# Kernel tuning notes

Hardware: AMD Instinct MI355X
Metric: run time of the kernel (lower is better)

The kernel has to match this reference:

```python
import jax, jax.numpy as jnp
import numpy as np

B, NQ, NK, D, H = 4, 2048, 2048, 1024, 16
HD = D // H


def setup_inputs() -> dict:
    key = jax.random.key(0)
    ks = jax.random.split(key, 11)
    s = 1.0 / np.sqrt(D)
    return {
        "q": jax.random.normal(ks[0], (B, NQ, D), jnp.float32),
        "k": jax.random.normal(ks[1], (B, NK, D), jnp.float32),
        "v": jax.random.normal(ks[2], (B, NK, D), jnp.float32),
        "Wq": jax.random.uniform(ks[3], (D, D), jnp.float32, -s, s),
        "bq": jax.random.uniform(ks[4], (D,), jnp.float32, -s, s),
        "Wk": jax.random.uniform(ks[5], (D, D), jnp.float32, -s, s),
        "bk": jax.random.uniform(ks[6], (D,), jnp.float32, -s, s),
        "Wv": jax.random.uniform(ks[7], (D, D), jnp.float32, -s, s),
        "bv": jax.random.uniform(ks[8], (D,), jnp.float32, -s, s),
        "Wo": jax.random.uniform(ks[9], (D, D), jnp.float32, -s, s),
        "bo": jax.random.uniform(ks[10], (D,), jnp.float32, -s, s),
    }


def reference(q, k, v, Wq, bq, Wk, bk, Wv, bv, Wo, bo):
    # Linear projections (torch Linear: x @ W.T + b), split into heads [B,H,N,HD]
    qh = (q @ Wq.T + bq).reshape(B, NQ, H, HD).transpose(0, 2, 1, 3)
    kh = (k @ Wk.T + bk).reshape(B, NK, H, HD).transpose(0, 2, 1, 3)
    vh = (v @ Wv.T + bv).reshape(B, NK, H, HD).transpose(0, 2, 1, 3)
    scores = jnp.einsum('bhqd,bhkd->bhqk', qh, kh) / np.sqrt(HD)  # [B,H,Nq,Nk]
    probs = jax.nn.softmax(scores, axis=-1)
    out = jnp.einsum('bhqk,bhkd->bhqd', probs, vh)
    out = out.transpose(0, 2, 1, 3).reshape(B, NQ, D)
    return out @ Wo.T + bo
```

## Files before the change

kernel.cpp:

```cpp
#include <hip/hip_runtime.h>
#include <hip/hip_bf16.h>
#include <cstdint>
#include <cstddef>


typedef __bf16 bf16x8 __attribute__((ext_vector_type(8)));
typedef float f32x4 __attribute__((ext_vector_type(4)));

#define BB 4
#define NQ 2048
#define NK 2048
#define DD 1024
#define HH 16
#define HD 64

#define QSCALE (0.125f * 1.4426950408889634f)

#if __has_builtin(__builtin_amdgcn_exp2f)
#define EXP2F(x) __builtin_amdgcn_exp2f(x)
#else
#define EXP2F(x) exp2f(x)
#endif

__device__ inline void gld_lds16(const void* g, void* lds) {
  __builtin_amdgcn_global_load_lds(
      (__attribute__((address_space(1))) unsigned int*)(g),
      (__attribute__((address_space(3))) unsigned int*)(lds),
      16, 0, 0);
}

__device__ inline bool probe_f32(const void* p) {
  const unsigned short* u = (const unsigned short*)p;
  int bad = 0;
#pragma unroll
  for (int i = 0; i < 64; ++i) {
    const int e = (u[2 * i] >> 7) & 0xFF;
    bad += (e > 0x8F) ? 1 : 0;
  }
  return bad >= 4;
}

__device__ inline bf16x8 cvt8(const float* src) {
  union { bf16x8 v; __hip_bfloat16 h[8]; } u;
#pragma unroll
  for (int j = 0; j < 8; ++j) u.h[j] = __float2bfloat16(src[j]);
  return u.v;
}

__global__ __launch_bounds__(256) void cvt_all(
    const void* __restrict__ q, const void* __restrict__ k,
    const void* __restrict__ v,
    const void* __restrict__ Wq, const void* __restrict__ Wk,
    const void* __restrict__ Wv, const void* __restrict__ Wo,
    __hip_bfloat16* __restrict__ qb, __hip_bfloat16* __restrict__ kb,
    __hip_bfloat16* __restrict__ vb, __hip_bfloat16* __restrict__ Wb) {
  const int bidx = blockIdx.x;
  const void* src; __hip_bfloat16* dst; size_t voff;
  if (bidx < 1536) {
    const int s = bidx >> 9;
    src = s == 0 ? q : (s == 1 ? k : v);
    dst = s == 0 ? qb : (s == 1 ? kb : vb);
    voff = (size_t)(bidx & 511) * 2048;
  } else {
    const int wi = (bidx - 1536) >> 6;
    src = wi == 0 ? Wq : (wi == 1 ? Wk : (wi == 2 ? Wv : Wo));
    dst = Wb + (size_t)wi * (DD * DD);
    voff = (size_t)((bidx - 1536) & 63) * 2048;
  }
  __shared__ int sflag;
  if (threadIdx.x == 0) sflag = probe_f32(src) ? 1 : 0;
  __syncthreads();
  const bool f32 = sflag != 0;
  const int t = threadIdx.x;
#pragma unroll
  for (int i = 0; i < 8; ++i) {
    const size_t j = voff + (size_t)i * 256 + t;
    if (f32) {
      union { f32x4 v2[2]; float f[8]; } u;
      const f32x4* s4 = (const f32x4*)src;
      u.v2[0] = s4[j * 2]; u.v2[1] = s4[j * 2 + 1];
      *(bf16x8*)(dst + j * 8) = cvt8(u.f);
    } else {
      *(f32x4*)(dst + j * 8) = ((const f32x4*)src)[j];
    }
  }
}

__global__ __launch_bounds__(256, 3) void gemm_fast(
    const __hip_bfloat16* __restrict__ qb, const __hip_bfloat16* __restrict__ kb,
    const __hip_bfloat16* __restrict__ vb, const __hip_bfloat16* __restrict__ At,
    const __hip_bfloat16* __restrict__ Wb,
    const void* __restrict__ bq, const void* __restrict__ bk,
    const void* __restrict__ bv, const void* __restrict__ bo,
    const void* __restrict__ WoOrig,
    void* __restrict__ Qp, void* __restrict__ Kp,
    void* __restrict__ Vt, void* __restrict__ Out, int cfg0) {
  __shared__ __align__(16) __hip_bfloat16 sA[2][128 * 32];
  __shared__ __align__(16) __hip_bfloat16 sB[2][128 * 32];
  const int t = threadIdx.x;
  const int wave = t >> 6, lane = t & 63;
  const int q4 = lane >> 4, c16 = lane & 15;
  const int wr = wave >> 1, wc = wave & 1;

  const int bid = blockIdx.x;
  const int xcd = bid & 7, idx = bid >> 3;
  const int z = idx >> 6;
  const int r6 = idx & 63;
  const int bm = xcd * 8 + (r6 >> 3);
  const int bn = r6 & 7;
  const int cfg = cfg0 + z;

  const __hip_bfloat16* A; const void* biasv; void* Cv; int mode; float scale = 1.f;
  if (cfg == 0)      { A = qb; biasv = bq; Cv = Qp; mode = 0; scale = QSCALE; }
  else if (cfg == 1) { A = kb; biasv = bk; Cv = Kp; mode = 0; }
  else if (cfg == 2) { A = vb; biasv = bv; Cv = Vt; mode = 1; }
  else               { A = At; biasv = bo; Cv = Out; mode = 2; }
  const __hip_bfloat16* Bm = Wb + (size_t)cfg * (DD * DD);

  const bool bias_f32 = probe_f32(biasv);
  const bool c_f32 = (mode == 2) && probe_f32(WoOrig);

  f32x4 acc[4][4];
#pragma unroll
  for (int i = 0; i < 4; ++i)
#pragma unroll
    for (int j = 0; j < 4; ++j) acc[i][j] = (f32x4){0.f, 0.f, 0.f, 0.f};

  const size_t baseA = (size_t)bm * 128 * DD;
  const size_t baseB = (size_t)bn * 128 * DD;
  const int po = ((q4) ^ (c16 & 3)) * 8;

  size_t offA[2], offB[2];
  int lslot[2];
#pragma unroll
  for (int i = 0; i < 2; ++i) {
    const int slot = i * 256 + t;
    const int row = slot >> 2, pg = (slot & 3) ^ (row & 3);
    lslot[i] = slot;
    offA[i] = baseA + (size_t)row * DD + pg * 8;
    offB[i] = baseB + (size_t)row * DD + pg * 8;
  }

#pragma unroll
  for (int i = 0; i < 2; ++i) {
    gld_lds16(A + offA[i], &sA[0][lslot[i] * 8]);
    gld_lds16(Bm + offB[i], &sB[0][lslot[i] * 8]);
  }
  __syncthreads();

  for (int it = 0; it < DD / 32; ++it) {
    const int p = it & 1;
    if (it + 1 < DD / 32) {
      const int koff = (it + 1) * 32;
#pragma unroll
      for (int i = 0; i < 2; ++i) {
        gld_lds16(A + offA[i] + koff, &sA[p ^ 1][lslot[i] * 8]);
        gld_lds16(Bm + offB[i] + koff, &sB[p ^ 1][lslot[i] * 8]);
      }
    }

    bf16x8 af[4], bfm[4];
#pragma unroll
    for (int rt = 0; rt < 4; ++rt)
      af[rt] = *(const bf16x8*)(&sA[p][0] + (wr * 64 + rt * 16 + c16) * 32 + po);
#pragma unroll
    for (int ct = 0; ct < 4; ++ct)
      bfm[ct] = *(const bf16x8*)(&sB[p][0] + (wc * 64 + ct * 16 + c16) * 32 + po);
#pragma unroll
    for (int rt = 0; rt < 4; ++rt)
#pragma unroll
      for (int ct = 0; ct < 4; ++ct)
        acc[rt][ct] = __builtin_amdgcn_mfma_f32_16x16x32_bf16(af[rt], bfm[ct],
                                                              acc[rt][ct], 0, 0, 0);

    __syncthreads();
  }

  const int row0 = bm * 128 + wr * 64 + q4 * 4;
  const int col0 = bn * 128 + wc * 64 + c16;
#pragma unroll
  for (int ct = 0; ct < 4; ++ct) {
    const int col = col0 + ct * 16;
    const float bvx = bias_f32 ? ((const float*)biasv)[col]
                               : __bfloat162float(((const __hip_bfloat16*)biasv)[col]);
#pragma unroll
    for (int rt = 0; rt < 4; ++rt) {
#pragma unroll
      for (int r = 0; r < 4; ++r) {
        const int row = row0 + rt * 16 + r;
        const float val = (acc[rt][ct][r] + bvx) * scale;
        if (mode == 1) {
          const int b = row >> 11, key = row & 2047;
          const int h = col >> 6, hd = col & 63;
          ((__hip_bfloat16*)Cv)[(size_t)((b * HH + h) * HD + hd) * NK + key] =
              __float2bfloat16(val);
        } else if (c_f32) {
          ((float*)Cv)[(size_t)row * DD + col] = val;
        } else {
          ((__hip_bfloat16*)Cv)[(size_t)row * DD + col] = __float2bfloat16(val);
        }
      }
    }
  }
}

__device__ inline void ld_slot(bool f32, const void* basep, size_t eoff,
                               f32x4& lo, f32x4& hi) {
  if (f32) {
    const f32x4* p = (const f32x4*)((const float*)basep + eoff);
    lo = p[0]; hi = p[1];
  } else {
    lo = *(const f32x4*)((const __hip_bfloat16*)basep + eoff);
  }
}

__device__ inline void st_slot(bool f32, __hip_bfloat16* dst, f32x4 lo, f32x4 hi) {
  if (f32) {
    union { f32x4 v[2]; float f[8]; } u;
    u.v[0] = lo; u.v[1] = hi;
    *(bf16x8*)dst = cvt8(u.f);
  } else {
    *(f32x4*)dst = lo;
  }
}

__global__ __launch_bounds__(256, 3) void gemm_mha(
    const void* __restrict__ qin, const void* __restrict__ kin,
    const void* __restrict__ vin, const void* __restrict__ ain,
    const void* __restrict__ Wq, const void* __restrict__ bq,
    const void* __restrict__ Wk, const void* __restrict__ bk,
    const void* __restrict__ Wv, const void* __restrict__ bv,
    const void* __restrict__ Wo, const void* __restrict__ bo,
    void* __restrict__ Qp, void* __restrict__ Kp,
    void* __restrict__ Vt, void* __restrict__ Out, int cfg0) {
  __shared__ __align__(16) __hip_bfloat16 sA[2][128 * 32];
  __shared__ __align__(16) __hip_bfloat16 sB[2][128 * 32];
  const int t = threadIdx.x;
  const int wave = t >> 6, lane = t & 63;
  const int q4 = lane >> 4, c16 = lane & 15;
  const int wr = wave >> 1, wc = wave & 1;

  const int bid = blockIdx.x;
  const int xcd = bid & 7, idx = bid >> 3;
  const int z = idx >> 6;
  const int r6 = idx & 63;
  const int bm = xcd * 8 + (r6 >> 3);
  const int bn = r6 & 7;
  const int cfg = cfg0 + z;

  const void *Av, *Bv, *biasv; void* Cv; int mode; float scale = 1.f;
  if (cfg == 0)      { Av = qin; Bv = Wq; biasv = bq; Cv = Qp; mode = 0; scale = QSCALE; }
  else if (cfg == 1) { Av = kin; Bv = Wk; biasv = bk; Cv = Kp; mode = 0; }
  else if (cfg == 2) { Av = vin; Bv = Wv; biasv = bv; Cv = Vt; mode = 1; }
  else               { Av = ain; Bv = Wo; biasv = bo; Cv = Out; mode = 2; }

  const bool a_f32 = probe_f32(Av);
  const bool b_f32 = probe_f32(Bv);
  const bool c_f32 = (mode == 2) && b_f32;

  f32x4 acc[4][4];
#pragma unroll
  for (int i = 0; i < 4; ++i)
#pragma unroll
    for (int j = 0; j < 4; ++j) acc[i][j] = (f32x4){0.f, 0.f, 0.f, 0.f};

  const size_t baseA = (size_t)bm * 128 * DD;
  const size_t baseB = (size_t)bn * 128 * DD;
  const int po = ((q4) ^ (c16 & 3)) * 8;

  size_t offA[2], offB[2];
  int lslot[2];
#pragma unroll
  for (int i = 0; i < 2; ++i) {
    const int slot = i * 256 + t;
    const int row = slot >> 2, pg = (slot & 3) ^ (row & 3);
    lslot[i] = slot;
    offA[i] = baseA + (size_t)row * DD + pg * 8;
    offB[i] = baseB + (size_t)row * DD + pg * 8;
  }

  f32x4 Alo[2], Ahi[2], Blo[2], Bhi[2];
#pragma unroll
  for (int i = 0; i < 2; ++i) {
    ld_slot(a_f32, Av, offA[i], Alo[i], Ahi[i]);
    ld_slot(b_f32, Bv, offB[i], Blo[i], Bhi[i]);
  }

  for (int k0 = 0, it = 0; k0 < DD; k0 += 32, ++it) {
    const int p = it & 1;
#pragma unroll
    for (int i = 0; i < 2; ++i) {
      st_slot(a_f32, &sA[p][lslot[i] * 8], Alo[i], Ahi[i]);
      st_slot(b_f32, &sB[p][lslot[i] * 8], Blo[i], Bhi[i]);
    }
    __syncthreads();

    if (k0 + 32 < DD) {
#pragma unroll
      for (int i = 0; i < 2; ++i) {
        ld_slot(a_f32, Av, offA[i] + k0 + 32, Alo[i], Ahi[i]);
        ld_slot(b_f32, Bv, offB[i] + k0 + 32, Blo[i], Bhi[i]);
      }
    }

    bf16x8 af[4], bfm[4];
#pragma unroll
    for (int rt = 0; rt < 4; ++rt)
      af[rt] = *(const bf16x8*)(&sA[p][0] + (wr * 64 + rt * 16 + c16) * 32 + po);
#pragma unroll
    for (int ct = 0; ct < 4; ++ct)
      bfm[ct] = *(const bf16x8*)(&sB[p][0] + (wc * 64 + ct * 16 + c16) * 32 + po);
#pragma unroll
    for (int rt = 0; rt < 4; ++rt)
#pragma unroll
      for (int ct = 0; ct < 4; ++ct)
        acc[rt][ct] = __builtin_amdgcn_mfma_f32_16x16x32_bf16(af[rt], bfm[ct],
                                                              acc[rt][ct], 0, 0, 0);
  }

  const int row0 = bm * 128 + wr * 64 + q4 * 4;
  const int col0 = bn * 128 + wc * 64 + c16;
#pragma unroll
  for (int ct = 0; ct < 4; ++ct) {
    const int col = col0 + ct * 16;
    const float bvx = b_f32 ? ((const float*)biasv)[col]
                            : __bfloat162float(((const __hip_bfloat16*)biasv)[col]);
#pragma unroll
    for (int rt = 0; rt < 4; ++rt) {
#pragma unroll
      for (int r = 0; r < 4; ++r) {
        const int row = row0 + rt * 16 + r;
        const float val = (acc[rt][ct][r] + bvx) * scale;
        if (mode == 1) {
          const int b = row >> 11, key = row & 2047;
          const int h = col >> 6, hd = col & 63;
          ((__hip_bfloat16*)Cv)[(size_t)((b * HH + h) * HD + hd) * NK + key] =
              __float2bfloat16(val);
        } else if (c_f32) {
          ((float*)Cv)[(size_t)row * DD + col] = val;
        } else {
          ((__hip_bfloat16*)Cv)[(size_t)row * DD + col] = __float2bfloat16(val);
        }
      }
    }
  }
}

__global__ __launch_bounds__(256, 3) void flash_attn(
    const __hip_bfloat16* Qp, const __hip_bfloat16* __restrict__ Kp,
    const __hip_bfloat16* __restrict__ Vt, __hip_bfloat16* Ao) {
  __shared__ __align__(16) __hip_bfloat16 sQP[128 * 64];
  __shared__ __align__(16) __hip_bfloat16 sK[2][64 * 64];
  __shared__ __align__(16) __hip_bfloat16 sV[2][64 * 64];

  const int t = threadIdx.x;
  const int wave = t >> 6, lane = t & 63;
  const int q4 = lane >> 4, c16 = lane & 15;
  const int xr = c16 & 7;

  const int bid = blockIdx.x;
  const int xcd = bid & 7, idx = bid >> 3;
  const int bh = xcd * 8 + (idx >> 4);
  const int qt = idx & 15;
  const int b = bh >> 4, h = bh & 15;

#pragma unroll
  for (int i = 0; i < 4; ++i) {
    const int slot = i * 256 + t;
    const int row = slot >> 3, pg = (slot & 7) ^ (row & 7);
    gld_lds16(Qp + ((size_t)(b * NQ + qt * 128 + row) * DD + h * 64 + pg * 8),
              sQP + slot * 8);
  }

  f32x4 o[2][4];
#pragma unroll
  for (int g = 0; g < 2; ++g)
#pragma unroll
    for (int i = 0; i < 4; ++i) o[g][i] = (f32x4){0.f, 0.f, 0.f, 0.f};
  float lp0 = 0.f, lp1 = 0.f;

  __syncthreads();

  bf16x8 aq[2][2];
#pragma unroll
  for (int qg = 0; qg < 2; ++qg)
#pragma unroll
    for (int ks = 0; ks < 2; ++ks)
      aq[qg][ks] = *(const bf16x8*)(sQP + (wave * 32 + qg * 16 + c16) * 64 +
                                    ((ks * 4 + q4) ^ xr) * 8);

#pragma unroll
  for (int i = 0; i < 2; ++i) {
    const int slot = i * 256 + t;
    const int row = slot >> 3, pg = (slot & 7) ^ (row & 7);
    gld_lds16(Kp + ((size_t)(b * NK + row) * DD + h * 64 + pg * 8),
              &sK[0][0] + slot * 8);
    gld_lds16(Vt + ((size_t)(bh * 64 + row) * NK + pg * 8),
              &sV[0][0] + slot * 8);
  }
  __syncthreads();

  const int prow0 = wave * 32 + c16;
  const int prow1 = wave * 32 + 16 + c16;

  for (int kt = 0; kt < NK / 64; ++kt) {
    const int p = kt & 1;
    if (kt + 1 < NK / 64) {
#pragma unroll
      for (int i = 0; i < 2; ++i) {
        const int slot = i * 256 + t;
        const int row = slot >> 3, pg = (slot & 7) ^ (row & 7);
        gld_lds16(Kp + ((size_t)(b * NK + (kt + 1) * 64 + row) * DD + h * 64 + pg * 8),
                  &sK[p ^ 1][0] + slot * 8);
        gld_lds16(Vt + ((size_t)(bh * 64 + row) * NK + (kt + 1) * 64 + pg * 8),
                  &sV[p ^ 1][0] + slot * 8);
      }
    }

    f32x4 s[2][4];
#pragma unroll
    for (int ct = 0; ct < 4; ++ct) {
      bf16x8 bk0 = *(const bf16x8*)(&sK[p][0] + (ct * 16 + c16) * 64 + ((0 + q4) ^ xr) * 8);
      bf16x8 bk1 = *(const bf16x8*)(&sK[p][0] + (ct * 16 + c16) * 64 + ((4 + q4) ^ xr) * 8);
#pragma unroll
      for (int qg = 0; qg < 2; ++qg) {
        f32x4 z = (f32x4){0.f, 0.f, 0.f, 0.f};
        z = __builtin_amdgcn_mfma_f32_16x16x32_bf16(bk0, aq[qg][0], z, 0, 0, 0);
        z = __builtin_amdgcn_mfma_f32_16x16x32_bf16(bk1, aq[qg][1], z, 0, 0, 0);
        s[qg][ct] = z;
      }
    }

#pragma unroll
    for (int qg = 0; qg < 2; ++qg) {
      const int prow = qg ? prow1 : prow0;
#pragma unroll
      for (int ct = 0; ct < 4; ++ct) {
        union { uint2 u; __hip_bfloat16 hx[4]; } pk;
#pragma unroll
        for (int r = 0; r < 4; ++r) {
          const float pe = EXP2F(s[qg][ct][r]);
          if (qg) lp1 += pe; else lp0 += pe;
          pk.hx[r] = __float2bfloat16(pe);
        }
        const int pc = (ct * 2 + (q4 >> 1)) ^ xr;
        *(uint2*)(sQP + prow * 64 + pc * 8 + (q4 & 1) * 4) = pk.u;
      }
    }

#pragma unroll
    for (int kk = 0; kk < 2; ++kk) {
      bf16x8 bvf[4];
#pragma unroll
      for (int ct2 = 0; ct2 < 4; ++ct2)
        bvf[ct2] = *(const bf16x8*)(&sV[p][0] + (ct2 * 16 + c16) * 64 + ((kk * 4 + q4) ^ xr) * 8);
      bf16x8 ap0 = *(const bf16x8*)(sQP + prow0 * 64 + ((kk * 4 + q4) ^ xr) * 8);
      bf16x8 ap1 = *(const bf16x8*)(sQP + prow1 * 64 + ((kk * 4 + q4) ^ xr) * 8);
#pragma unroll
      for (int ct2 = 0; ct2 < 4; ++ct2) {
        o[0][ct2] = __builtin_amdgcn_mfma_f32_16x16x32_bf16(ap0, bvf[ct2], o[0][ct2], 0, 0, 0);
        o[1][ct2] = __builtin_amdgcn_mfma_f32_16x16x32_bf16(ap1, bvf[ct2], o[1][ct2], 0, 0, 0);
      }
    }

    __syncthreads();
  }

  float lr[2][4];
#pragma unroll
  for (int qg = 0; qg < 2; ++qg) {
    float lq = (qg ? lp1 : lp0);
    lq += __shfl_xor(lq, 16, 64);
    lq += __shfl_xor(lq, 32, 64);
    const float linv = 1.f / lq;
#pragma unroll
    for (int r = 0; r < 4; ++r) lr[qg][r] = __shfl(linv, q4 * 4 + r, 64);
  }

#pragma unroll
  for (int qg = 0; qg < 2; ++qg)
#pragma unroll
    for (int ct2 = 0; ct2 < 4; ++ct2)
#pragma unroll
      for (int r = 0; r < 4; ++r) {
        const size_t row = (size_t)(b * NQ + qt * 128 + wave * 32 + qg * 16 + q4 * 4 + r);
        Ao[row * DD + h * 64 + ct2 * 16 + c16] = __float2bfloat16(o[qg][ct2][r] * lr[qg][r]);
      }
}

extern "C" void kernel_launch(void* const* d_in, const int* in_sizes, int n_in,
                              void* d_out, int out_size, void* d_ws, size_t ws_size,
                              hipStream_t stream) {
  const void* q  = d_in[0];
  const void* k  = d_in[1];
  const void* v  = d_in[2];
  const void* Wq = d_in[3];
  const void* bq = d_in[4];
  const void* Wk = d_in[5];
  const void* bk = d_in[6];
  const void* Wv = d_in[7];
  const void* bv = d_in[8];
  const void* Wo = d_in[9];
  const void* bo = d_in[10];

  const size_t MP = (size_t)BB * NQ;
  const size_t MAT = MP * DD;
  __hip_bfloat16* Qp = (__hip_bfloat16*)d_ws;
  __hip_bfloat16* Vt = Qp + MAT;
  __hip_bfloat16* Kp = (__hip_bfloat16*)d_out;
  __hip_bfloat16* At = Qp;

  const size_t NEED = (4 * MAT + 4 * (size_t)(DD * DD)) * sizeof(__hip_bfloat16);
  if (ws_size >= NEED) {
    __hip_bfloat16* kb = Vt + MAT;
    __hip_bfloat16* vb = kb + MAT;
    __hip_bfloat16* Wb = vb + MAT;
    __hip_bfloat16* qb = (__hip_bfloat16*)d_out + MAT;

    cvt_all<<<dim3(1792), 256, 0, stream>>>(q, k, v, Wq, Wk, Wv, Wo,
                                            qb, kb, vb, Wb);
    gemm_fast<<<dim3(1536), 256, 0, stream>>>(qb, kb, vb, At, Wb,
                                              bq, bk, bv, bo, Wo,
                                              Qp, Kp, Vt, d_out, 0);
    flash_attn<<<dim3(1024), 256, 0, stream>>>(Qp, Kp, Vt, At);
    gemm_fast<<<dim3(512), 256, 0, stream>>>(qb, kb, vb, At, Wb,
                                             bq, bk, bv, bo, Wo,
                                             Qp, Kp, Vt, d_out, 3);
  } else {
    gemm_mha<<<dim3(1536), 256, 0, stream>>>(
        q, k, v, At, Wq, bq, Wk, bk, Wv, bv, Wo, bo, Qp, Kp, Vt, d_out, 0);
    flash_attn<<<dim3(1024), 256, 0, stream>>>(Qp, Kp, Vt, At);
    gemm_mha<<<dim3(512), 256, 0, stream>>>(
        q, k, v, At, Wq, bq, Wk, bk, Wv, bv, Wo, bo, Qp, Kp, Vt, d_out, 3);
  }
}
```

Baseline: 392.2 us.

## Replace double-buffered K32 GEMM loop with single-buffered K64 tiles

The projection GEMM's main loop moves from a double-buffered LDS pipeline with a 32-wide K step to a single buffer holding a 64-wide K tile. The XOR swizzle widens from 4 to 8 column groups to match. This halves the number of outer iterations and barriers per tile while keeping LDS usage the same. In exchange, global-to-LDS loads no longer overlap with MFMA work, since each tile is loaded and synchronized before compute begins.

```diff
diff --git a/kernel.cpp b/kernel.cpp
--- a/kernel.cpp
+++ b/kernel.cpp
@@ -95,11 +95,12 @@
     const void* __restrict__ WoOrig,
     void* __restrict__ Qp, void* __restrict__ Kp,
     void* __restrict__ Vt, void* __restrict__ Out, int cfg0) {
-  __shared__ __align__(16) __hip_bfloat16 sA[2][128 * 32];
-  __shared__ __align__(16) __hip_bfloat16 sB[2][128 * 32];
+  __shared__ __align__(16) __hip_bfloat16 sA[128 * 64];
+  __shared__ __align__(16) __hip_bfloat16 sB[128 * 64];
   const int t = threadIdx.x;
   const int wave = t >> 6, lane = t & 63;
   const int q4 = lane >> 4, c16 = lane & 15;
+  const int xr = c16 & 7;
   const int wr = wave >> 1, wc = wave & 1;
 
   const int bid = blockIdx.x;
@@ -128,52 +129,46 @@
 
   const size_t baseA = (size_t)bm * 128 * DD;
   const size_t baseB = (size_t)bn * 128 * DD;
-  const int po = ((q4) ^ (c16 & 3)) * 8;
-
-  size_t offA[2], offB[2];
-  int lslot[2];
-#pragma unroll
-  for (int i = 0; i < 2; ++i) {
+
+  size_t offA[4], offB[4];
+  int lslot[4];
+#pragma unroll
+  for (int i = 0; i < 4; ++i) {
     const int slot = i * 256 + t;
-    const int row = slot >> 2, pg = (slot & 3) ^ (row & 3);
+    const int row = slot >> 3, pg = (slot & 7) ^ (row & 7);
     lslot[i] = slot;
     offA[i] = baseA + (size_t)row * DD + pg * 8;
     offB[i] = baseB + (size_t)row * DD + pg * 8;
   }
 
-#pragma unroll
-  for (int i = 0; i < 2; ++i) {
-    gld_lds16(A + offA[i], &sA[0][lslot[i] * 8]);
-    gld_lds16(Bm + offB[i], &sB[0][lslot[i] * 8]);
-  }
-  __syncthreads();
-
-  for (int it = 0; it < DD / 32; ++it) {
-    const int p = it & 1;
-    if (it + 1 < DD / 32) {
-      const int koff = (it + 1) * 32;
-#pragma unroll
-      for (int i = 0; i < 2; ++i) {
-        gld_lds16(A + offA[i] + koff, &sA[p ^ 1][lslot[i] * 8]);
-        gld_lds16(Bm + offB[i] + koff, &sB[p ^ 1][lslot[i] * 8]);
-      }
-    }
-
-    bf16x8 af[4], bfm[4];
-#pragma unroll
-    for (int rt = 0; rt < 4; ++rt)
-      af[rt] = *(const bf16x8*)(&sA[p][0] + (wr * 64 + rt * 16 + c16) * 32 + po);
-#pragma unroll
-    for (int ct = 0; ct < 4; ++ct)
-      bfm[ct] = *(const bf16x8*)(&sB[p][0] + (wc * 64 + ct * 16 + c16) * 32 + po);
-#pragma unroll
-    for (int rt = 0; rt < 4; ++rt)
+  for (int k0 = 0; k0 < DD; k0 += 64) {
+    __syncthreads();
+#pragma unroll
+    for (int i = 0; i < 4; ++i)
+      gld_lds16(A + offA[i] + k0, sA + lslot[i] * 8);
+#pragma unroll
+    for (int i = 0; i < 4; ++i)
+      gld_lds16(Bm + offB[i] + k0, sB + lslot[i] * 8);
+    __syncthreads();
+
+#pragma unroll
+    for (int ks = 0; ks < 2; ++ks) {
+      bf16x8 af[4], bfm[4];
+#pragma unroll
+      for (int rt = 0; rt < 4; ++rt)
+        af[rt] = *(const bf16x8*)(sA + (wr * 64 + rt * 16 + c16) * 64 +
+                                  ((ks * 4 + q4) ^ xr) * 8);
 #pragma unroll
       for (int ct = 0; ct < 4; ++ct)
-        acc[rt][ct] = __builtin_amdgcn_mfma_f32_16x16x32_bf16(af[rt], bfm[ct],
-                                                              acc[rt][ct], 0, 0, 0);
-
-    __syncthreads();
+        bfm[ct] = *(const bf16x8*)(sB + (wc * 64 + ct * 16 + c16) * 64 +
+                                   ((ks * 4 + q4) ^ xr) * 8);
+#pragma unroll
+      for (int rt = 0; rt < 4; ++rt)
+#pragma unroll
+        for (int ct = 0; ct < 4; ++ct)
+          acc[rt][ct] = __builtin_amdgcn_mfma_f32_16x16x32_bf16(af[rt], bfm[ct],
+                                                                acc[rt][ct], 0, 0, 0);
+    }
   }
 
   const int row0 = bm * 128 + wr * 64 + q4 * 4;
```

After: 386.1 us. Within noise of the previous version (-1.6%).
